# Optimization experiments

Measured on AMD Instinct MI355X. Metric: run time of the kernel, lower is better.

## Reference

```python
import jax, jax.numpy as jnp
import numpy as np

B, T, C = 4, 2048, 1024
NUM_HEAD = 16
HEAD_DIM = C // NUM_HEAD


def setup_inputs() -> dict:
    key = jax.random.key(0)
    k = jax.random.split(key, 5)
    scale = 1.0 / np.sqrt(C)
    return {
        "hidden_states": jax.random.normal(k[0], (B, T, C), dtype=jnp.float32),
        "w_qkv": jax.random.normal(k[1], (C, 3 * C), dtype=jnp.float32) * scale,
        "b_qkv": jnp.zeros((3 * C,), dtype=jnp.float32),
        "w_o": jax.random.normal(k[2], (C, C), dtype=jnp.float32) * scale,
        "b_o": jnp.zeros((C,), dtype=jnp.float32),
    }


def reference(hidden_states, w_qkv, b_qkv, w_o, b_o):
    Bb, Tt, Cc = hidden_states.shape
    scaling = HEAD_DIM ** -0.5
    qkv = hidden_states @ w_qkv + b_qkv  # [B,T,3C]
    q, k, v = jnp.split(qkv, 3, axis=-1)
    # [B,T,C] -> [B,H,T,Dh]
    def heads(x):
        return x.reshape(Bb, Tt, NUM_HEAD, HEAD_DIM).transpose(0, 2, 1, 3)
    q, k, v = heads(q), heads(k), heads(v)
    scores = jnp.einsum("bhqd,bhkd->bhqk", q, k) * scaling  # [B,H,T,T]
    causal = jnp.tril(jnp.ones((Tt, Tt), dtype=bool))
    scores = jnp.where(causal, scores, -jnp.inf)
    attn = jax.nn.softmax(scores, axis=-1)
    out = jnp.einsum("bhqk,bhkd->bhqd", attn, v)  # [B,H,T,Dh]
    out = out.transpose(0, 2, 1, 3).reshape(Bb, Tt, Cc)
    return out @ w_o + b_o
```

## Files before the change

### kernel.cpp

```cpp
#include <hip/hip_runtime.h>
#include <hip/hip_bf16.h>

#define B_ 4
#define T_ 2048
#define C_ 1024
#define NH 16
#define HD 64
#define M_TOK (B_*T_)

typedef unsigned short u16;
typedef __bf16 bf16x8 __attribute__((ext_vector_type(8)));
typedef short short8 __attribute__((ext_vector_type(8)));
typedef float f32x4 __attribute__((ext_vector_type(4)));
typedef unsigned u32x4 __attribute__((ext_vector_type(4)));
typedef unsigned short u16x4 __attribute__((ext_vector_type(4)));

static __device__ __forceinline__ u16 f2bf(float f) {
    union { float f; unsigned u; } a; a.f = f;
    unsigned u = a.u;
    u = u + 0x7fff + ((u >> 16) & 1);
    return (u16)(u >> 16);
}

static __device__ __forceinline__ unsigned cvtpk(float lo, float hi) {
    unsigned r;
    asm("v_cvt_pk_bf16_f32 %0, %1, %2" : "=v"(r) : "v"(lo), "v"(hi));
    return r;
}

static __device__ __forceinline__ f32x4 mfma16(short8 a, short8 b, f32x4 c) {
    return __builtin_amdgcn_mfma_f32_16x16x32_bf16(
        __builtin_bit_cast(bf16x8, a), __builtin_bit_cast(bf16x8, b), c, 0, 0, 0);
}

#define GLOAD16(gp, lp) __builtin_amdgcn_global_load_lds( \
    (const __attribute__((address_space(1))) unsigned*)(const void*)(gp), \
    (__attribute__((address_space(3))) unsigned*)(void*)(lp), 16, 0, 0)

__global__ void convert_x(const float* __restrict__ src, u16* __restrict__ dst, int n4) {
    int i = blockIdx.x * blockDim.x + threadIdx.x;
    if (i < n4) {
        const float4 v = *(const float4*)(src + (size_t)i * 4);
        u16x4 o;
        o[0] = f2bf(v.x); o[1] = f2bf(v.y); o[2] = f2bf(v.z); o[3] = f2bf(v.w);
        *(u16x4*)(dst + (size_t)i * 4) = o;
    }
}

__global__ void transpose_bf16(const float* __restrict__ src, u16* __restrict__ dst,
                               int rows, int cols) {
    __shared__ float tile[32][33];
    const int c0 = blockIdx.x * 32, r0 = blockIdx.y * 32;
    const int tx = threadIdx.x, ty = threadIdx.y;
    #pragma unroll
    for (int j = ty; j < 32; j += 8)
        tile[j][tx] = src[(size_t)(r0 + j) * cols + c0 + tx];
    __syncthreads();
    #pragma unroll
    for (int j = ty; j < 32; j += 8)
        dst[(size_t)(c0 + j) * rows + r0 + tx] = f2bf(tile[tx][j]);
}

template<int OUT_BF16>
__global__ __launch_bounds__(256) void gemm_bt(
    const u16* __restrict__ A,
    const u16* __restrict__ Bt,
    const float* __restrict__ bias,
    u16* __restrict__ Cb, float* __restrict__ Cf,
    int M, int N, int K, int scale_ncols, float scale)
{
    __shared__ u16 Al[128 * 32];
    __shared__ u16 Bl[128 * 32];
    const int tid  = threadIdx.x;
    const int lane = tid & 63;
    const int w    = tid >> 6;
    const int wr   = w >> 1, wc = w & 1;
    const int bm   = blockIdx.y * 128, bn = blockIdx.x * 128;

    f32x4 acc[4][4] = {};

    const int srow = (w << 4) + (lane >> 2);
    const int scol = (lane & 3) * 8;
    const u16* gA0 = A  + (size_t)(bm + srow) * K + scol;
    const u16* gA1 = gA0 + (size_t)64 * K;
    const u16* gB0 = Bt + (size_t)(bn + srow) * K + scol;
    const u16* gB1 = gB0 + (size_t)64 * K;
    u16* lA0 = &Al[(w << 4) * 32];
    u16* lA1 = &Al[(64 + (w << 4)) * 32];
    u16* lB0 = &Bl[(w << 4) * 32];
    u16* lB1 = &Bl[(64 + (w << 4)) * 32];

    const int fr = lane & 15;
    const int fk = (lane >> 4) * 8;

    for (int k0 = 0; k0 < K; k0 += 32) {
        GLOAD16(gA0 + k0, lA0);
        GLOAD16(gA1 + k0, lA1);
        GLOAD16(gB0 + k0, lB0);
        GLOAD16(gB1 + k0, lB1);
        __syncthreads();

        short8 af[4], bfr[4];
        #pragma unroll
        for (int m = 0; m < 4; m++) af[m]  = *(const short8*)&Al[(wr * 64 + m * 16 + fr) * 32 + fk];
        #pragma unroll
        for (int n = 0; n < 4; n++) bfr[n] = *(const short8*)&Bl[(wc * 64 + n * 16 + fr) * 32 + fk];
        #pragma unroll
        for (int m = 0; m < 4; m++)
            #pragma unroll
            for (int n = 0; n < 4; n++)
                acc[m][n] = mfma16(af[m], bfr[n], acc[m][n]);
        __syncthreads();
    }

    const int r0 = (lane >> 4) * 4;
    #pragma unroll
    for (int m = 0; m < 4; m++) {
        #pragma unroll
        for (int i = 0; i < 4; i++) {
            const int grow = bm + wr * 64 + m * 16 + r0 + i;
            #pragma unroll
            for (int n = 0; n < 4; n++) {
                const int gcol = bn + wc * 64 + n * 16 + fr;
                float v = acc[m][n][i] + bias[gcol];
                if (gcol < scale_ncols) v *= scale;
                if (OUT_BF16) Cb[(size_t)grow * N + gcol] = f2bf(v);
                else          Cf[(size_t)grow * N + gcol] = v;
            }
        }
    }
}

__global__ __launch_bounds__(256, 4) void attn_fwd(
    const u16* __restrict__ qkv,
    u16* __restrict__ out)
{
    __shared__ u16 Kl[2][64][72];
    __shared__ u16 Vp[2][64 * 64];

    const int tid  = threadIdx.x;
    const int lane = tid & 63;
    const int wv   = tid >> 6;
    const int bid  = blockIdx.x;
    const int head = bid >> 4;
    const int b = head >> 4, h = head & 15;
    const int qt = 15 - (((bid & 15) + ((bid >> 8) << 2)) & 15);
    const int tok0 = b * T_;
    const int q0 = qt * 128 + wv * 32;
    const int fr = lane & 15;
    const int fg = lane >> 4;
    const int fk = fg * 8;

    short8 aq[2][2];
    #pragma unroll
    for (int rg = 0; rg < 2; rg++) {
        const u16* qp = qkv + (size_t)(tok0 + q0 + rg * 16 + fr) * (3 * C_) + h * HD;
        aq[rg][0] = *(const short8*)(qp + fk);
        aq[rg][1] = *(const short8*)(qp + 32 + fk);
    }

    f32x4 oacc[2][4] = {};
    float mrow[2] = { -INFINITY, -INFINITY };
    float lsum[2] = { 0.f, 0.f };

    const int kvrk = tid >> 2;
    const int kck  = (tid & 3) * 8;
    const int kvrv  = lane;
    const int dbase = wv * 16;
    const int s_  = (kvrv & 32) | (((kvrv >> 2) & 3) << 3) | (((kvrv >> 4) & 1) << 2) | (kvrv & 3);
    const int vgcol = s_ >> 3;
    const int vso   = s_ & 7;

    short8 kreg0, kreg1, vreg0, vreg1;

#define LOAD_TILE(kt_) { \
    const u16* kpk = qkv + (size_t)(tok0 + (kt_) * 64 + kvrk) * (3 * C_) + C_ + h * HD + kck; \
    kreg0 = *(const short8*)kpk;        kreg1 = *(const short8*)(kpk + 32); \
    const u16* kpv = qkv + (size_t)(tok0 + (kt_) * 64 + kvrv) * (3 * C_) + 2 * C_ + h * HD + dbase; \
    vreg0 = *(const short8*)kpv;        vreg1 = *(const short8*)(kpv + 8); }

#define WRITE_TILE(bf) { \
    *(short8*)&Kl[bf][kvrk][kck]      = kreg0; \
    *(short8*)&Kl[bf][kvrk][kck + 32] = kreg1; \
    _Pragma("unroll") \
    for (int j = 0; j < 8; j++) { \
        Vp[bf][(dbase + j)     * 64 + (((vgcol ^ j) & 7) << 3) + vso] = (u16)vreg0[j]; \
        Vp[bf][(dbase + 8 + j) * 64 + (((vgcol ^ j) & 7) << 3) + vso] = (u16)vreg1[j]; } }

    LOAD_TILE(0); WRITE_TILE(0);

    const int ntiles = 2 * qt + 2;
    #pragma unroll 1
    for (int kt = 0; kt < ntiles; ++kt) {
        const int cb = kt & 1;
        const bool havenext = (kt + 1 < ntiles);
        if (havenext) LOAD_TILE(kt + 1);
        __syncthreads();

        if (kt * 64 <= q0 + 31) {
            #pragma unroll
            for (int rg = 0; rg < 2; rg++) {
                f32x4 s[4] = {};
                __builtin_amdgcn_s_setprio(1);
                #pragma unroll
                for (int fc = 0; fc < 4; fc++) {
                    const short8 k0 = *(const short8*)&Kl[cb][fc * 16 + fr][fk];
                    const short8 k1 = *(const short8*)&Kl[cb][fc * 16 + fr][32 + fk];
                    s[fc] = mfma16(k0, aq[rg][0], s[fc]);
                    s[fc] = mfma16(k1, aq[rg][1], s[fc]);
                }
                __builtin_amdgcn_s_setprio(0);

                const int qg = q0 + rg * 16 + fr;
                if (kt * 64 + 63 > q0 + rg * 16) {
                    #pragma unroll
                    for (int fc = 0; fc < 4; fc++)
                        #pragma unroll
                        for (int i = 0; i < 4; i++)
                            if (kt * 64 + fc * 16 + fg * 4 + i > qg) s[fc][i] = -INFINITY;
                }
                float pmax = -INFINITY;
                #pragma unroll
                for (int fc = 0; fc < 4; fc++)
                    #pragma unroll
                    for (int i = 0; i < 4; i++)
                        pmax = fmaxf(pmax, s[fc][i]);
                pmax = fmaxf(pmax, __shfl_xor(pmax, 16, 64));
                pmax = fmaxf(pmax, __shfl_xor(pmax, 32, 64));

                if (!__all(pmax <= mrow[rg] + 11.0f)) {
                    const float mnew = fmaxf(mrow[rg], pmax);
                    const float alpha = __builtin_amdgcn_exp2f(mrow[rg] - mnew);
                    mrow[rg] = mnew;
                    lsum[rg] *= alpha;
                    float av[4];
                    #pragma unroll
                    for (int i = 0; i < 4; i++) av[i] = __shfl(alpha, (fg << 2) + i, 64);
                    #pragma unroll
                    for (int df = 0; df < 4; df++)
                        #pragma unroll
                        for (int i = 0; i < 4; i++) oacc[rg][df][i] *= av[i];
                }
                const float mref = mrow[rg];

                float ps = 0.f;
                u32x4 wl[2];
                #pragma unroll
                for (int fc = 0; fc < 4; fc++) {
                    const float p0 = __builtin_amdgcn_exp2f(s[fc][0] - mref);
                    const float p1 = __builtin_amdgcn_exp2f(s[fc][1] - mref);
                    const float p2 = __builtin_amdgcn_exp2f(s[fc][2] - mref);
                    const float p3 = __builtin_amdgcn_exp2f(s[fc][3] - mref);
                    ps += (p0 + p1) + (p2 + p3);
                    wl[fc >> 1][(fc & 1) * 2 + 0] = cvtpk(p0, p1);
                    wl[fc >> 1][(fc & 1) * 2 + 1] = cvtpk(p2, p3);
                }
                ps += __shfl_xor(ps, 16, 64);
                ps += __shfl_xor(ps, 32, 64);
                lsum[rg] += ps;

                __builtin_amdgcn_s_setprio(1);
                #pragma unroll
                for (int c = 0; c < 2; c++) {
                    const short8 ap = __builtin_bit_cast(short8, wl[c]);
                    #pragma unroll
                    for (int df = 0; df < 4; df++) {
                        const short8 bv = *(const short8*)
                            &Vp[cb][(df * 16 + fr) * 64 + ((((c << 2) + fg) ^ (fr & 7)) << 3)];
                        oacc[rg][df] = mfma16(ap, bv, oacc[rg][df]);
                    }
                }
                __builtin_amdgcn_s_setprio(0);
            }
        }
        if (havenext) WRITE_TILE(!cb);
    }

    #pragma unroll
    for (int rg = 0; rg < 2; rg++) {
        #pragma unroll
        for (int i = 0; i < 4; i++) {
            const float li = __shfl(lsum[rg], (fg << 2) + i, 64);
            const float inv = 1.f / li;
            const int tokn = tok0 + q0 + rg * 16 + fg * 4 + i;
            #pragma unroll
            for (int df = 0; df < 4; df++)
                out[(size_t)tokn * C_ + h * HD + df * 16 + fr] = f2bf(oacc[rg][df][i] * inv);
        }
    }
#undef LOAD_TILE
#undef WRITE_TILE
}

extern "C" void kernel_launch(void* const* d_in, const int* in_sizes, int n_in,
                              void* d_out, int out_size, void* d_ws, size_t ws_size,
                              hipStream_t stream) {
    const float* hs    = (const float*)d_in[0];
    const float* w_qkv = (const float*)d_in[1];
    const float* b_qkv = (const float*)d_in[2];
    const float* w_o   = (const float*)d_in[3];
    const float* b_o   = (const float*)d_in[4];
    float* out = (float*)d_out;

    u16* Xb    = (u16*)d_ws;
    u16* WqkvT = Xb    + (size_t)M_TOK * C_;
    u16* WoT   = WqkvT + (size_t)3 * C_ * C_;
    u16* QKV   = WoT   + (size_t)C_ * C_;
    u16* AO    = QKV   + (size_t)M_TOK * 3 * C_;

    {
        const int n4 = M_TOK * C_ / 4;
        convert_x<<<(n4 + 255) / 256, 256, 0, stream>>>(hs, Xb, n4);
        dim3 tb(32, 8);
        transpose_bf16<<<dim3(3 * C_ / 32, C_ / 32), tb, 0, stream>>>(w_qkv, WqkvT, C_, 3 * C_);
        transpose_bf16<<<dim3(C_ / 32, C_ / 32), tb, 0, stream>>>(w_o, WoT, C_, C_);
    }

    gemm_bt<1><<<dim3(3 * C_ / 128, M_TOK / 128), 256, 0, stream>>>(
        Xb, WqkvT, b_qkv, QKV, nullptr, M_TOK, 3 * C_, C_, C_, 0.125f * 1.44269504f);

    attn_fwd<<<dim3(T_ / 128 * B_ * NH), 256, 0, stream>>>(QKV, AO);

    gemm_bt<0><<<dim3(C_ / 128, M_TOK / 128), 256, 0, stream>>>(
        AO, WoT, b_o, nullptr, out, M_TOK, C_, C_, 0, 1.f);
}
```

Baseline: 228.5 us.

## Deepen GEMM K-tile to 64 with XOR-swizzled LDS and remap attention block order

The GEMM now stages a 64-wide K slice per iteration instead of 32, loading A and B tiles with an XOR swizzle on 16-byte chunks to avoid LDS bank conflicts. This halves the barrier count per K and doubles MFMA work between syncs, at the cost of twice the shared memory per block. Separately, the attention kernel's block-to-(head, q-tile) mapping changes so that consecutive blocks walk heads first and q-tiles in increasing order. That drops the previous heavy-first reverse ordering used for causal load balancing.

```diff
diff --git a/kernel.cpp b/kernel.cpp
--- a/kernel.cpp
+++ b/kernel.cpp
@@ -69,8 +69,8 @@
     u16* __restrict__ Cb, float* __restrict__ Cf,
     int M, int N, int K, int scale_ncols, float scale)
 {
-    __shared__ u16 Al[128 * 32];
-    __shared__ u16 Bl[128 * 32];
+    __shared__ u16 Al[128 * 64];
+    __shared__ u16 Bl[128 * 64];
     const int tid  = threadIdx.x;
     const int lane = tid & 63;
     const int w    = tid >> 6;
@@ -79,37 +79,43 @@
 
     f32x4 acc[4][4] = {};
 
-    const int srow = (w << 4) + (lane >> 2);
-    const int scol = (lane & 3) * 8;
-    const u16* gA0 = A  + (size_t)(bm + srow) * K + scol;
-    const u16* gA1 = gA0 + (size_t)64 * K;
-    const u16* gB0 = Bt + (size_t)(bn + srow) * K + scol;
-    const u16* gB1 = gB0 + (size_t)64 * K;
-    u16* lA0 = &Al[(w << 4) * 32];
-    u16* lA1 = &Al[(64 + (w << 4)) * 32];
-    u16* lB0 = &Bl[(w << 4) * 32];
-    u16* lB1 = &Bl[(64 + (w << 4)) * 32];
+    const int srow = tid >> 3;
+    const int schk = ((tid & 7) ^ (srow & 7)) * 8;
+    const u16* gA = A  + (size_t)(bm + srow) * K + schk;
+    const u16* gB = Bt + (size_t)(bn + srow) * K + schk;
+    u16* lA = &Al[(w << 3) * 64];
+    u16* lB = &Bl[(w << 3) * 64];
 
     const int fr = lane & 15;
-    const int fk = (lane >> 4) * 8;
-
-    for (int k0 = 0; k0 < K; k0 += 32) {
-        GLOAD16(gA0 + k0, lA0);
-        GLOAD16(gA1 + k0, lA1);
-        GLOAD16(gB0 + k0, lB0);
-        GLOAD16(gB1 + k0, lB1);
+    const int fg = lane >> 4;
+
+    for (int k0 = 0; k0 < K; k0 += 64) {
+        #pragma unroll
+        for (int inst = 0; inst < 4; inst++) {
+            GLOAD16(gA + (size_t)(inst * 32) * K + k0, lA + inst * 32 * 64);
+            GLOAD16(gB + (size_t)(inst * 32) * K + k0, lB + inst * 32 * 64);
+        }
         __syncthreads();
 
-        short8 af[4], bfr[4];
         #pragma unroll
-        for (int m = 0; m < 4; m++) af[m]  = *(const short8*)&Al[(wr * 64 + m * 16 + fr) * 32 + fk];
-        #pragma unroll
-        for (int n = 0; n < 4; n++) bfr[n] = *(const short8*)&Bl[(wc * 64 + n * 16 + fr) * 32 + fk];
-        #pragma unroll
-        for (int m = 0; m < 4; m++)
-            #pragma unroll
-            for (int n = 0; n < 4; n++)
-                acc[m][n] = mfma16(af[m], bfr[n], acc[m][n]);
+        for (int ks = 0; ks < 2; ks++) {
+            short8 af[4], bfr[4];
+            #pragma unroll
+            for (int m = 0; m < 4; m++) {
+                const int rh = wr * 64 + m * 16 + fr;
+                af[m] = *(const short8*)&Al[rh * 64 + ((((ks << 2) | fg) ^ (fr & 7)) << 3)];
+            }
+            #pragma unroll
+            for (int n = 0; n < 4; n++) {
+                const int rh = wc * 64 + n * 16 + fr;
+                bfr[n] = *(const short8*)&Bl[rh * 64 + ((((ks << 2) | fg) ^ (fr & 7)) << 3)];
+            }
+            #pragma unroll
+            for (int m = 0; m < 4; m++)
+                #pragma unroll
+                for (int n = 0; n < 4; n++)
+                    acc[m][n] = mfma16(af[m], bfr[n], acc[m][n]);
+        }
         __syncthreads();
     }
 
@@ -142,9 +148,9 @@
     const int lane = tid & 63;
     const int wv   = tid >> 6;
     const int bid  = blockIdx.x;
-    const int head = bid >> 4;
+    const int head = bid & 63;
     const int b = head >> 4, h = head & 15;
-    const int qt = 15 - (((bid & 15) + ((bid >> 8) << 2)) & 15);
+    const int qt = bid >> 6;
     const int tok0 = b * T_;
     const int q0 = qt * 128 + wv * 32;
     const int fr = lane & 15;
```

Measured after the change: 202.1 us, median of 3. 11.6% less time.
